# Optimization experiments

Hardware: AMD Instinct MI355X
Metric: run time of the kernel (lower is better)

Reference implementation:

```python
import jax, jax.numpy as jnp
import numpy as np

K = 7           # kernel_size
PAD = K // 2    # padding (stride=dilation=1 path)


def setup_inputs() -> dict:
    key = jax.random.key(0)
    ks = jax.random.split(key, 5)
    B, Cin, H, W = 8, 256, 96, 96
    A = 128  # attn_channels
    x = jax.random.normal(ks[0], (B, Cin, H, W), dtype=jnp.float32)
    w_q = jax.random.normal(ks[1], (A, Cin), dtype=jnp.float32) * 0.05
    w_k = jax.random.normal(ks[2], (A, Cin), dtype=jnp.float32) * 0.05
    rel_h = jax.random.normal(ks[3], (A // 2, 1, 1, K, 1), dtype=jnp.float32)
    rel_w = jax.random.normal(ks[4], (A // 2, 1, 1, 1, K), dtype=jnp.float32)
    return {"x": x, "w_q": w_q, "w_k": w_k, "rel_h": rel_h, "rel_w": rel_w}


def reference(x, w_q, w_k, rel_h, rel_w):
    # x: [B, Cin, H, W]; w_q/w_k: [A, Cin] (1x1 convs); rel_h/rel_w: [A/2,1,1,K,1]/[A/2,1,1,1,K]
    B, Cin, H, W = x.shape
    A = w_q.shape[0]
    half = A // 2

    q = jnp.einsum('bchw,oc->bohw', x, w_q)  # [B, A, H, W]
    k = jnp.einsum('bchw,oc->bohw', x, w_k)  # [B, A, H, W]
    k_pad = jnp.pad(k, ((0, 0), (0, 0), (PAD, PAD), (PAD, PAD)))

    # Positional-bias contribution: window key at offset (ki,kj) has rel_h[:,ki]
    # added to its first A/2 channels and rel_w[:,kj] added to its second half.
    # Since sim sums over all channels (group matmul + sum over groups), the
    # bias terms factor out of the window gather:
    rh = rel_h.reshape(half, K)  # [A/2, K]
    rw = rel_w.reshape(half, K)  # [A/2, K]
    bias_h = jnp.einsum('bchw,ck->bhwk', q[:, :half], rh)  # [B,H,W,K]
    bias_w = jnp.einsum('bchw,ck->bhwk', q[:, half:], rw)  # [B,H,W,K]

    # Main term: sim[b,h,w,ki,kj] = sum_c q[b,c,h,w] * k_pad[b,c,h+ki,w+kj].
    # Fixed K*K loop over kernel offsets (not over data dims); avoids the
    # redundant [B,A,H,W,K,K] unfolded tensor the torch code materializes.
    sim_main = jnp.stack([
        jnp.stack([
            jnp.einsum('bchw,bchw->bhw', q, k_pad[:, :, i:i + H, j:j + W])
            for j in range(K)
        ], axis=-1)
        for i in range(K)
    ], axis=-2)  # [B, H, W, K, K]

    return sim_main + bias_h[..., :, None] + bias_w[..., None, :]
```

## Files before the change

kernel.cpp:

```cpp
#include <hip/hip_runtime.h>
#include <stdint.h>

#define CIN 256
#define NH 96
#define NW 96
#define HWP (NH*NW)
#define NA 128
#define KS 7
#define PAD 3

typedef __attribute__((ext_vector_type(8))) short  short8;
typedef __attribute__((ext_vector_type(8))) unsigned short u16x8;
typedef __attribute__((ext_vector_type(4))) unsigned short u16x4;
typedef __attribute__((ext_vector_type(4))) float  f32x4;

__device__ __forceinline__ unsigned short f2bf(float f) {
    unsigned int u = __float_as_uint(f);
    unsigned int r = (u + 0x7fffu + ((u >> 16) & 1u)) >> 16;
    return (unsigned short)r;
}
__device__ __forceinline__ unsigned int pk2(float a, float b) {
    return ((unsigned int)f2bf(b) << 16) | f2bf(a);
}
__device__ __forceinline__ int swsl(int slot, int row) { return slot ^ (row & 15); }

__device__ __forceinline__ f32x4 mfma16(short8 a, short8 b, f32x4 c) {
    return __builtin_amdgcn_mfma_f32_16x16x32_bf16(a, b, c, 0, 0, 0);
}

#define BN 128
#define BK 32
#define NKSTEPS (CIN/BK)
#define APITCH 40
#define XPITCH 40

__global__ __launch_bounds__(512) void qk_gemm(
    const float* __restrict__ x, const float* __restrict__ wq,
    const float* __restrict__ wk, unsigned int* __restrict__ y, int b0)
{
    __shared__ unsigned short Al[2][256*APITCH];
    __shared__ unsigned short Xl[2][BN*XPITCH];

    const int tid = threadIdx.x;
    const int bl  = blockIdx.x / (HWP/BN);
    const int pt  = blockIdx.x % (HWP/BN);
    const int b   = b0 + bl;
    const int p0  = pt * BN;

    const int lane = tid & 63;
    const int wid  = tid >> 6;
    const int wm   = wid >> 1;
    const int wn   = wid & 1;
    const int l15  = lane & 15;
    const int l4   = lane >> 4;

    const int ar  = tid >> 1;
    const int ac0 = (tid & 1) * 16;
    const float* wrow = (ar < NA) ? (wq + (size_t)ar * CIN)
                                  : (wk + (size_t)(ar - NA) * CIN);

    const int xp   = tid & 127;
    const int cq2  = (tid >> 7) * 2;
    const float* xb = x + (size_t)b * CIN * HWP + p0 + xp;

    float a_stage[16];
    float x_stage[8];

    f32x4 acc[4][4];
    #pragma unroll
    for (int m = 0; m < 4; ++m)
        #pragma unroll
        for (int n = 0; n < 4; ++n)
            acc[m][n] = (f32x4){0.f, 0.f, 0.f, 0.f};

    auto LOAD = [&](int kt) {
        const f32x4* s4 = reinterpret_cast<const f32x4*>(wrow + kt*BK + ac0);
        #pragma unroll
        for (int i = 0; i < 4; ++i) {
            f32x4 v = s4[i];
            a_stage[i*4+0] = v[0]; a_stage[i*4+1] = v[1];
            a_stage[i*4+2] = v[2]; a_stage[i*4+3] = v[3];
        }
        #pragma unroll
        for (int i = 0; i < 2; ++i) {
            const int c = kt*BK + (cq2 + i)*4;
            #pragma unroll
            for (int j = 0; j < 4; ++j)
                x_stage[i*4+j] = xb[(size_t)(c + j) * HWP];
        }
    };

    auto WRITE = [&](int bi) {
        u16x8 v0, v1;
        #pragma unroll
        for (int j = 0; j < 8; ++j) { v0[j] = f2bf(a_stage[j]); v1[j] = f2bf(a_stage[8+j]); }
        *reinterpret_cast<u16x8*>(&Al[bi][ar*APITCH + ac0    ]) = v0;
        *reinterpret_cast<u16x8*>(&Al[bi][ar*APITCH + ac0 + 8]) = v1;
        #pragma unroll
        for (int i = 0; i < 2; ++i) {
            u16x4 xv;
            #pragma unroll
            for (int j = 0; j < 4; ++j) xv[j] = f2bf(x_stage[i*4+j]);
            *reinterpret_cast<u16x4*>(&Xl[bi][xp*XPITCH + (cq2 + i)*4]) = xv;
        }
    };

    auto COMPUTE = [&](int bi) {
        short8 aF[4], bF[4];
        #pragma unroll
        for (int m = 0; m < 4; ++m)
            aF[m] = *reinterpret_cast<const short8*>(
                &Al[bi][(wm*64 + m*16 + l15)*APITCH + l4*8]);
        #pragma unroll
        for (int n = 0; n < 4; ++n)
            bF[n] = *reinterpret_cast<const short8*>(
                &Xl[bi][(wn*64 + n*16 + l15)*XPITCH + l4*8]);
        #pragma unroll
        for (int m = 0; m < 4; ++m)
            #pragma unroll
            for (int n = 0; n < 4; ++n)
                acc[m][n] = mfma16(aF[m], bF[n], acc[m][n]);
    };

    LOAD(0);
    WRITE(0);
    for (int kt = 0; kt < NKSTEPS; ++kt) {
        if (kt + 1 < NKSTEPS) LOAD(kt + 1);
        __syncthreads();
        COMPUTE(kt & 1);
        if (kt + 1 < NKSTEPS) WRITE((kt + 1) & 1);
    }

    __syncthreads();
    unsigned int* buf = reinterpret_cast<unsigned int*>(&Al[0][0]) + wid * (64*20);
    unsigned int* yB  = y + (size_t)bl * (HWP*128);
    #pragma unroll
    for (int hm = 0; hm < 2; ++hm) {
        #pragma unroll
        for (int mm = 0; mm < 2; ++mm) {
            const int m = hm*2 + mm;
            #pragma unroll
            for (int n = 0; n < 4; ++n) {
                const int px  = n*16 + l15;
                const int jcl = mm*8 + l4*2;
                uint2 d;
                d.x = pk2(acc[m][n][0], acc[m][n][1]);
                d.y = pk2(acc[m][n][2], acc[m][n][3]);
                *reinterpret_cast<uint2*>(&buf[px*20 + jcl]) = d;
            }
        }
        __syncthreads();
        #pragma unroll
        for (int pass = 0; pass < 4; ++pass) {
            const int pxl = (lane >> 2) + pass*16;
            const int sl  = lane & 3;
            uint4 v = *reinterpret_cast<const uint4*>(&buf[pxl*20 + sl*4]);
            const int p = p0 + wn*64 + pxl;
            *reinterpret_cast<uint4*>(&yB[(size_t)p*128 + wm*32 + hm*16 + sl*4]) = v;
        }
        __syncthreads();
    }
}

__global__ __launch_bounds__(384) void sim_mfma(
    const unsigned int* __restrict__ y, const float* __restrict__ relh,
    const float* __restrict__ relw, float* __restrict__ out, int b0, int nwg)
{
    __shared__ unsigned int qL[96*64];
    __shared__ unsigned int kL[112*64];
    __shared__ unsigned int bB[16*64];
    __shared__ float extL[6][16*33];
    __shared__ float biasL[6][16*17];

    const int orig = blockIdx.x;
    const int qq = nwg >> 3, rr = nwg & 7;
    const int xcd = orig & 7, off = orig >> 3;
    const int wg = (xcd < rr ? xcd*(qq+1) : rr*(qq+1) + (xcd-rr)*qq) + off;
    const int bl = wg / NH;
    const int h  = wg % NH;

    const int tid  = threadIdx.x;
    const int wid  = tid >> 6;
    const int lane = tid & 63;
    const int l15  = lane & 15, l4 = lane >> 4;
    const int m0   = wid * 16;

    const unsigned int* yb = y + (size_t)bl * (HWP*128);

    {
        const int sl = tid & 15, pxb = tid >> 4;
        #pragma unroll
        for (int pass = 0; pass < 4; ++pass) {
            const int p = pxb + pass*24;
            uint4 v = *reinterpret_cast<const uint4*>(yb + (size_t)(h*NW + p)*128 + sl*4);
            *reinterpret_cast<uint4*>(&qL[p*64 + swsl(sl, p)*4]) = v;
        }
    }
    if (tid < 256) {
        const int sl = tid & 15, n = tid >> 4;
        uint4 v = {0u,0u,0u,0u};
        if (n < 14) {
            #pragma unroll
            for (int u = 0; u < 4; ++u) {
                const int jc = sl*4 + u;
                float lo = 0.f, hi = 0.f;
                if (n < 7) {
                    if (jc < 32) { lo = relh[(2*jc)*KS + n]; hi = relh[(2*jc+1)*KS + n]; }
                } else {
                    if (jc >= 32) { const int c = 2*jc - 64;
                        lo = relw[c*KS + (n-7)]; hi = relw[(c+1)*KS + (n-7)]; }
                }
                ((unsigned int*)&v)[u] = pk2(lo, hi);
            }
        }
        *reinterpret_cast<uint4*>(&bB[n*64 + swsl(sl, n)*4]) = v;
    }
    __syncthreads();

    short8 aF[4];
    #pragma unroll
    for (int ks = 0; ks < 4; ++ks)
        aF[ks] = *reinterpret_cast<const short8*>(
            &qL[(m0 + l15)*64 + swsl(ks*4 + l4, l15)*4]);

    {
        f32x4 bacc = {0.f,0.f,0.f,0.f};
        #pragma unroll
        for (int ks = 0; ks < 4; ++ks) {
            short8 bF = *reinterpret_cast<const short8*>(
                &bB[l15*64 + swsl(ks*4 + l4, l15)*4]);
            bacc = mfma16(aF[ks], bF, bacc);
        }
        #pragma unroll
        for (int i = 0; i < 4; ++i)
            biasL[wid][(l4*4 + i)*17 + l15] = bacc[i];
    }

    for (int ki = 0; ki < KS; ++ki) {
        __syncthreads();
        const int r = h + ki - PAD;
        {
            const int sl = tid & 15, gib = tid >> 4;
            #pragma unroll
            for (int pass = 0; pass < 5; ++pass) {
                const int g = gib + pass*24;
                if (g < 112) {
                    uint4 v = {0u,0u,0u,0u};
                    const int p = g - PAD;
                    if ((unsigned)r < (unsigned)NH && (unsigned)p < (unsigned)NW)
                        v = *reinterpret_cast<const uint4*>(
                            yb + (size_t)(r*NW + p)*128 + 64 + sl*4);
                    *reinterpret_cast<uint4*>(&kL[g*64 + swsl(sl, g)*4]) = v;
                }
            }
        }
        __syncthreads();

        f32x4 a0 = {0.f,0.f,0.f,0.f}, a1 = {0.f,0.f,0.f,0.f};
        #pragma unroll
        for (int ks = 0; ks < 4; ++ks) {
            short8 b0f = *reinterpret_cast<const short8*>(
                &kL[(m0 + l15)*64      + swsl(ks*4 + l4, l15)*4]);
            short8 b1f = *reinterpret_cast<const short8*>(
                &kL[(m0 + 16 + l15)*64 + swsl(ks*4 + l4, l15)*4]);
            a0 = mfma16(aF[ks], b0f, a0);
            a1 = mfma16(aF[ks], b1f, a1);
        }
        #pragma unroll
        for (int i = 0; i < 4; ++i) {
            extL[wid][(l4*4 + i)*33 + l15]      = a0[i];
            extL[wid][(l4*4 + i)*33 + 16 + l15] = a1[i];
        }
        __syncthreads();

        {
            const int px = l15;
            const float* eb = extL[wid];
            const float* bb = biasL[wid];
            const float bki = bb[px*17 + ki];
            const size_t ob = ((size_t)((b0 + bl)*NH + h)*NW + m0 + px)*(KS*KS) + ki*KS;
            const int kj1 = l4;
            out[ob + kj1] = eb[px*33 + px + kj1] + bki + bb[px*17 + 7 + kj1];
            if (l4 < 3) {
                const int kj2 = l4 + 4;
                out[ob + kj2] = eb[px*33 + px + kj2] + bki + bb[px*17 + 7 + kj2];
            }
        }
    }
}

extern "C" void kernel_launch(void* const* d_in, const int* in_sizes, int n_in,
                              void* d_out, int out_size, void* d_ws, size_t ws_size,
                              hipStream_t stream)
{
    const float* x  = (const float*)d_in[0];
    const float* wq = (const float*)d_in[1];
    const float* wk = (const float*)d_in[2];
    const float* rh = (const float*)d_in[3];
    const float* rw = (const float*)d_in[4];
    float* out = (float*)d_out;

    const int B = 8;
    const size_t perBatch = (size_t)HWP * 128 * sizeof(unsigned int);
    int bc = (ws_size >= perBatch) ? (int)(ws_size / perBatch) : 1;
    if (bc > B) bc = B;

    unsigned int* y = (unsigned int*)d_ws;

    for (int b0 = 0; b0 < B; b0 += bc) {
        const int nb = (B - b0 < bc) ? (B - b0) : bc;
        qk_gemm<<<dim3(nb * (HWP/BN)), dim3(512), 0, stream>>>(x, wq, wk, y, b0);
        const int nwg = nb * NH;
        sim_mfma<<<dim3(nwg), dim3(384), 0, stream>>>(y, rh, rw, out, b0, nwg);
    }
}
```

Baseline: 176.4 us.

## Prepack bf16 weights, stream them via global_load_lds, read sim operands from global

A new small kernel converts the q/k projection weights to bf16 once, in a swizzled layout. The GEMM then copies each weight tile straight into LDS with global_load_lds, removing the per-block fp32 load and conversion work. Its epilogue drops block-wide barriers because each wave uses its own staging buffer. The sim kernel no longer stages q and the padded k rows in shared memory. It loads MFMA operands directly from global memory with bounds masks, which removes the per-row block barriers but relies on cache hits for less coalesced loads. Whether the direct-to-LDS copies are properly waited on before the barrier is left to the compiler.

Result: faster. 165.3 us (-6.3%).

```diff
diff --git a/kernel.cpp b/kernel.cpp
--- a/kernel.cpp
+++ b/kernel.cpp
@@ -9,8 +9,8 @@
 #define KS 7
 #define PAD 3
 
+typedef unsigned int u32;
 typedef __attribute__((ext_vector_type(8))) short  short8;
-typedef __attribute__((ext_vector_type(8))) unsigned short u16x8;
 typedef __attribute__((ext_vector_type(4))) unsigned short u16x4;
 typedef __attribute__((ext_vector_type(4))) float  f32x4;
 
@@ -27,19 +27,47 @@
 __device__ __forceinline__ f32x4 mfma16(short8 a, short8 b, f32x4 c) {
     return __builtin_amdgcn_mfma_f32_16x16x32_bf16(a, b, c, 0, 0, 0);
 }
+__device__ __forceinline__ short8 as_s8(uint4 v) {
+    union { uint4 u; short8 s; } cv; cv.u = v; return cv.s;
+}
+__device__ __forceinline__ void gl_lds16(const u32* g, u32* l) {
+    __builtin_amdgcn_global_load_lds(
+        (const __attribute__((address_space(1))) u32*)g,
+        (__attribute__((address_space(3))) u32*)l, 16, 0, 0);
+}
+
+__global__ __launch_bounds__(256) void wprep(
+    const float* __restrict__ wq, const float* __restrict__ wk,
+    u32* __restrict__ preW)
+{
+    const int id  = blockIdx.x * 256 + threadIdx.x;
+    const int kt  = id >> 10;
+    const int rem = id & 1023;
+    const int row = rem >> 2;
+    const int s   = rem & 3;
+    const int g   = s ^ (row & 3);
+    const float* wr = (row < NA) ? (wq + (size_t)row * CIN)
+                                 : (wk + (size_t)(row - NA) * CIN);
+    const float* src = wr + kt*32 + g*8;
+    uint4 d;
+    d.x = pk2(src[0], src[1]);
+    d.y = pk2(src[2], src[3]);
+    d.z = pk2(src[4], src[5]);
+    d.w = pk2(src[6], src[7]);
+    *reinterpret_cast<uint4*>(preW + (size_t)id * 4) = d;
+}
 
 #define BN 128
 #define BK 32
 #define NKSTEPS (CIN/BK)
-#define APITCH 40
-#define XPITCH 40
+#define ADW 4096
+#define XDW 2560
 
 __global__ __launch_bounds__(512) void qk_gemm(
-    const float* __restrict__ x, const float* __restrict__ wq,
-    const float* __restrict__ wk, unsigned int* __restrict__ y, int b0)
+    const float* __restrict__ x, const u32* __restrict__ preW,
+    u32* __restrict__ y, int b0)
 {
-    __shared__ unsigned short Al[2][256*APITCH];
-    __shared__ unsigned short Xl[2][BN*XPITCH];
+    __shared__ u32 arena[13312];
 
     const int tid = threadIdx.x;
     const int bl  = blockIdx.x / (HWP/BN);
@@ -53,19 +81,13 @@
     const int wn   = wid & 1;
     const int l15  = lane & 15;
     const int l4   = lane >> 4;
-
-    const int ar  = tid >> 1;
-    const int ac0 = (tid & 1) * 16;
-    const float* wrow = (ar < NA) ? (wq + (size_t)ar * CIN)
-                                  : (wk + (size_t)(ar - NA) * CIN);
+    const int xr   = (l4 ^ (l15 & 3)) << 2;
 
     const int xp   = tid & 127;
     const int cq2  = (tid >> 7) * 2;
     const float* xb = x + (size_t)b * CIN * HWP + p0 + xp;
 
-    float a_stage[16];
     float x_stage[8];
-
     f32x4 acc[4][4];
     #pragma unroll
     for (int m = 0; m < 4; ++m)
@@ -73,14 +95,13 @@
         for (int n = 0; n < 4; ++n)
             acc[m][n] = (f32x4){0.f, 0.f, 0.f, 0.f};
 
-    auto LOAD = [&](int kt) {
-        const f32x4* s4 = reinterpret_cast<const f32x4*>(wrow + kt*BK + ac0);
-        #pragma unroll
-        for (int i = 0; i < 4; ++i) {
-            f32x4 v = s4[i];
-            a_stage[i*4+0] = v[0]; a_stage[i*4+1] = v[1];
-            a_stage[i*4+2] = v[2]; a_stage[i*4+3] = v[3];
-        }
+    auto GLLDSA = [&](int kt, int bi) {
+        const u32* src = preW + kt*ADW + wid*512 + lane*4;
+        u32* dst = arena + bi*ADW + wid*512;
+        gl_lds16(src, dst);
+        gl_lds16(src + 256, dst + 256);
+    };
+    auto LOADX = [&](int kt) {
         #pragma unroll
         for (int i = 0; i < 2; ++i) {
             const int c = kt*BK + (cq2 + i)*4;
@@ -89,32 +110,28 @@
                 x_stage[i*4+j] = xb[(size_t)(c + j) * HWP];
         }
     };
-
-    auto WRITE = [&](int bi) {
-        u16x8 v0, v1;
-        #pragma unroll
-        for (int j = 0; j < 8; ++j) { v0[j] = f2bf(a_stage[j]); v1[j] = f2bf(a_stage[8+j]); }
-        *reinterpret_cast<u16x8*>(&Al[bi][ar*APITCH + ac0    ]) = v0;
-        *reinterpret_cast<u16x8*>(&Al[bi][ar*APITCH + ac0 + 8]) = v1;
+    auto WRITEX = [&](int bi) {
+        unsigned short* Xu = (unsigned short*)(arena + 8192 + bi*XDW);
         #pragma unroll
         for (int i = 0; i < 2; ++i) {
             u16x4 xv;
             #pragma unroll
             for (int j = 0; j < 4; ++j) xv[j] = f2bf(x_stage[i*4+j]);
-            *reinterpret_cast<u16x4*>(&Xl[bi][xp*XPITCH + (cq2 + i)*4]) = xv;
+            *reinterpret_cast<u16x4*>(Xu + xp*40 + (cq2 + i)*4) = xv;
         }
     };
-
     auto COMPUTE = [&](int bi) {
+        const u32* Ab = arena + bi*ADW;
+        const unsigned short* Xu = (const unsigned short*)(arena + 8192 + bi*XDW);
         short8 aF[4], bF[4];
         #pragma unroll
         for (int m = 0; m < 4; ++m)
             aF[m] = *reinterpret_cast<const short8*>(
-                &Al[bi][(wm*64 + m*16 + l15)*APITCH + l4*8]);
+                Ab + (wm*64 + m*16 + l15)*16 + xr);
         #pragma unroll
         for (int n = 0; n < 4; ++n)
             bF[n] = *reinterpret_cast<const short8*>(
-                &Xl[bi][(wn*64 + n*16 + l15)*XPITCH + l4*8]);
+                Xu + (wn*64 + n*16 + l15)*40 + l4*8);
         #pragma unroll
         for (int m = 0; m < 4; ++m)
             #pragma unroll
@@ -122,18 +139,17 @@
                 acc[m][n] = mfma16(aF[m], bF[n], acc[m][n]);
     };
 
-    LOAD(0);
-    WRITE(0);
+    GLLDSA(0, 0); LOADX(0); WRITEX(0);
     for (int kt = 0; kt < NKSTEPS; ++kt) {
-        if (kt + 1 < NKSTEPS) LOAD(kt + 1);
         __syncthreads();
+        if (kt + 1 < NKSTEPS) { GLLDSA(kt + 1, (kt + 1) & 1); LOADX(kt + 1); }
         COMPUTE(kt & 1);
-        if (kt + 1 < NKSTEPS) WRITE((kt + 1) & 1);
+        if (kt + 1 < NKSTEPS) WRITEX((kt + 1) & 1);
     }
 
     __syncthreads();
-    unsigned int* buf = reinterpret_cast<unsigned int*>(&Al[0][0]) + wid * (64*20);
-    unsigned int* yB  = y + (size_t)bl * (HWP*128);
+    u32* buf = arena + wid * 1280;
+    u32* yB  = y + (size_t)bl * (HWP*128);
     #pragma unroll
     for (int hm = 0; hm < 2; ++hm) {
         #pragma unroll
@@ -149,7 +165,6 @@
                 *reinterpret_cast<uint2*>(&buf[px*20 + jcl]) = d;
             }
         }
-        __syncthreads();
         #pragma unroll
         for (int pass = 0; pass < 4; ++pass) {
             const int pxl = (lane >> 2) + pass*16;
@@ -158,17 +173,14 @@
             const int p = p0 + wn*64 + pxl;
             *reinterpret_cast<uint4*>(&yB[(size_t)p*128 + wm*32 + hm*16 + sl*4]) = v;
         }
-        __syncthreads();
     }
 }
 
 __global__ __launch_bounds__(384) void sim_mfma(
-    const unsigned int* __restrict__ y, const float* __restrict__ relh,
+    const u32* __restrict__ y, const float* __restrict__ relh,
     const float* __restrict__ relw, float* __restrict__ out, int b0, int nwg)
 {
-    __shared__ unsigned int qL[96*64];
-    __shared__ unsigned int kL[112*64];
-    __shared__ unsigned int bB[16*64];
+    __shared__ u32 bB[16*64];
     __shared__ float extL[6][16*33];
     __shared__ float biasL[6][16*17];
 
@@ -185,17 +197,8 @@
     const int l15  = lane & 15, l4 = lane >> 4;
     const int m0   = wid * 16;
 
-    const unsigned int* yb = y + (size_t)bl * (HWP*128);
-
-    {
-        const int sl = tid & 15, pxb = tid >> 4;
-        #pragma unroll
-        for (int pass = 0; pass < 4; ++pass) {
-            const int p = pxb + pass*24;
-            uint4 v = *reinterpret_cast<const uint4*>(yb + (size_t)(h*NW + p)*128 + sl*4);
-            *reinterpret_cast<uint4*>(&qL[p*64 + swsl(sl, p)*4]) = v;
-        }
-    }
+    const u32* yb = y + (size_t)bl * (HWP*128);
+
     if (tid < 256) {
         const int sl = tid & 15, n = tid >> 4;
         uint4 v = {0u,0u,0u,0u};
@@ -218,10 +221,10 @@
     __syncthreads();
 
     short8 aF[4];
+    const u32* qrow = yb + (size_t)(h*NW + m0 + l15) * 128;
     #pragma unroll
     for (int ks = 0; ks < 4; ++ks)
-        aF[ks] = *reinterpret_cast<const short8*>(
-            &qL[(m0 + l15)*64 + swsl(ks*4 + l4, l15)*4]);
+        aF[ks] = as_s8(*reinterpret_cast<const uint4*>(qrow + (ks*4 + l4)*4));
 
     {
         f32x4 bacc = {0.f,0.f,0.f,0.f};
@@ -236,56 +239,38 @@
             biasL[wid][(l4*4 + i)*17 + l15] = bacc[i];
     }
 
+    const int pA = m0 + l15 - PAD;
+    const int pB = m0 + 16 + l15 - PAD;
+    const bool okA = (unsigned)pA < (unsigned)NW;
+    const bool okB = (unsigned)pB < (unsigned)NW;
+
     for (int ki = 0; ki < KS; ++ki) {
-        __syncthreads();
         const int r = h + ki - PAD;
-        {
-            const int sl = tid & 15, gib = tid >> 4;
-            #pragma unroll
-            for (int pass = 0; pass < 5; ++pass) {
-                const int g = gib + pass*24;
-                if (g < 112) {
-                    uint4 v = {0u,0u,0u,0u};
-                    const int p = g - PAD;
-                    if ((unsigned)r < (unsigned)NH && (unsigned)p < (unsigned)NW)
-                        v = *reinterpret_cast<const uint4*>(
-                            yb + (size_t)(r*NW + p)*128 + 64 + sl*4);
-                    *reinterpret_cast<uint4*>(&kL[g*64 + swsl(sl, g)*4]) = v;
-                }
-            }
-        }
-        __syncthreads();
-
+        const bool rok = (unsigned)r < (unsigned)NH;
+        const u32* rbase = yb + (size_t)r * NW * 128 + 64;
         f32x4 a0 = {0.f,0.f,0.f,0.f}, a1 = {0.f,0.f,0.f,0.f};
         #pragma unroll
         for (int ks = 0; ks < 4; ++ks) {
-            short8 b0f = *reinterpret_cast<const short8*>(
-                &kL[(m0 + l15)*64      + swsl(ks*4 + l4, l15)*4]);
-            short8 b1f = *reinterpret_cast<const short8*>(
-                &kL[(m0 + 16 + l15)*64 + swsl(ks*4 + l4, l15)*4]);
-            a0 = mfma16(aF[ks], b0f, a0);
-            a1 = mfma16(aF[ks], b1f, a1);
+            uint4 v0 = {0u,0u,0u,0u}, v1 = {0u,0u,0u,0u};
+            if (rok && okA)
+                v0 = *reinterpret_cast<const uint4*>(rbase + (size_t)pA*128 + (ks*4 + l4)*4);
+            if (rok && okB)
+                v1 = *reinterpret_cast<const uint4*>(rbase + (size_t)pB*128 + (ks*4 + l4)*4);
+            a0 = mfma16(aF[ks], as_s8(v0), a0);
+            a1 = mfma16(aF[ks], as_s8(v1), a1);
         }
         #pragma unroll
         for (int i = 0; i < 4; ++i) {
             extL[wid][(l4*4 + i)*33 + l15]      = a0[i];
             extL[wid][(l4*4 + i)*33 + 16 + l15] = a1[i];
         }
-        __syncthreads();
-
-        {
-            const int px = l15;
-            const float* eb = extL[wid];
-            const float* bb = biasL[wid];
-            const float bki = bb[px*17 + ki];
-            const size_t ob = ((size_t)((b0 + bl)*NH + h)*NW + m0 + px)*(KS*KS) + ki*KS;
-            const int kj1 = l4;
-            out[ob + kj1] = eb[px*33 + px + kj1] + bki + bb[px*17 + 7 + kj1];
-            if (l4 < 3) {
-                const int kj2 = l4 + 4;
-                out[ob + kj2] = eb[px*33 + px + kj2] + bki + bb[px*17 + 7 + kj2];
-            }
-        }
+        const float* eb = extL[wid];
+        const float* bb = biasL[wid];
+        const float bki = bb[l15*17 + ki];
+        const size_t ob = ((size_t)((b0 + bl)*NH + h)*NW + m0 + l15)*(KS*KS) + ki*KS;
+        out[ob + l4] = eb[l15*33 + l15 + l4] + bki + bb[l15*17 + 7 + l4];
+        if (l4 < 3)
+            out[ob + l4 + 4] = eb[l15*33 + l15 + l4 + 4] + bki + bb[l15*17 + 11 + l4];
     }
 }
 
@@ -301,15 +286,18 @@
     float* out = (float*)d_out;
 
     const int B = 8;
-    const size_t perBatch = (size_t)HWP * 128 * sizeof(unsigned int);
-    int bc = (ws_size >= perBatch) ? (int)(ws_size / perBatch) : 1;
+    u32* preW = (u32*)d_ws;
+    u32* y    = (u32*)d_ws + 32768;
+    const size_t perBatch = (size_t)HWP * 128 * sizeof(u32);
+    size_t avail = ws_size > 131072 ? ws_size - 131072 : 0;
+    int bc = (avail >= perBatch) ? (int)(avail / perBatch) : 1;
     if (bc > B) bc = B;
 
-    unsigned int* y = (unsigned int*)d_ws;
+    wprep<<<dim3(32), dim3(256), 0, stream>>>(wq, wk, preW);
 
     for (int b0 = 0; b0 < B; b0 += bc) {
         const int nb = (B - b0 < bc) ? (B - b0) : bc;
-        qk_gemm<<<dim3(nb * (HWP/BN)), dim3(512), 0, stream>>>(x, wq, wk, y, b0);
+        qk_gemm<<<dim3(nb * (HWP/BN)), dim3(512), 0, stream>>>(x, preW, y, b0);
         const int nwg = nb * NH;
         sim_mfma<<<dim3(nwg), dim3(384), 0, stream>>>(y, rh, rw, out, b0, nwg);
     }
```
